# Optimization experiments

Hardware: AMD Instinct MI355X
Metric: run time of the kernel (lower is better)

The kernel has to match this reference:

```python
import jax, jax.numpy as jnp
import numpy as np

VOCAB, EMB, ATT = 100000, 128, 128
N_CODES, N_ANC = 100000, 8

def setup_inputs() -> dict:
    key = jax.random.key(0)
    k1, k2, k3, k4, k5 = jax.random.split(key, 5)
    return {
        "W_emb": jax.random.normal(k1, (VOCAB, EMB), dtype=jnp.float32),
        "W_attention": jax.random.normal(k2, (2 * EMB, ATT), dtype=jnp.float32) * 0.05,
        "b_attention": jnp.zeros((ATT,), dtype=jnp.float32),
        "v_attention": jax.random.normal(k3, (ATT,), dtype=jnp.float32) * 0.05,
        "leaves": jax.random.randint(k4, (N_CODES, N_ANC), 0, VOCAB, dtype=jnp.int64),
        "ancestors": jax.random.randint(k5, (N_CODES, N_ANC), 0, VOCAB, dtype=jnp.int64),
    }

def reference(W_emb, W_attention, b_attention, v_attention, leaves, ancestors):
    # gather: [N, A, E] each
    leave_emb = W_emb[leaves]
    anc_emb = W_emb[ancestors]
    attention_input = jnp.concatenate((leave_emb, anc_emb), axis=2)  # [N, A, 2E]
    mlp = jnp.tanh(jnp.einsum('nae,ed->nad', attention_input, W_attention) + b_attention)
    pre_attention = jnp.einsum('nad,d->na', mlp, v_attention)  # [N, A]
    attn = jax.nn.softmax(pre_attention, axis=1)
    # attention-weighted sum over ancestors: [N, E]
    return jnp.einsum('nae,na->ne', anc_emb, attn)
```

## Files before the change

### kernel.cpp

```cpp
#include <hip/hip_runtime.h>
#include <hip/hip_bf16.h>
#include <hip/hip_fp8.h>

#define VOCAB  100000
#define EMB    128
#define NCODES 100000
#define NANC   8

typedef __attribute__((ext_vector_type(8))) short    short8;
typedef __attribute__((ext_vector_type(4))) float    float4v;
typedef __attribute__((ext_vector_type(2))) float    floatx2;
typedef __attribute__((ext_vector_type(4))) unsigned uint4v;
typedef __attribute__((ext_vector_type(2))) __bf16   bf16x2;

__device__ __forceinline__ ushort f2bf(float x) {
    unsigned u = __float_as_uint(x);
    u += 0x7fffu + ((u >> 16) & 1u);
    return (ushort)(u >> 16);
}
__device__ __forceinline__ float bf2f(ushort h) {
    return __uint_as_float((unsigned)h << 16);
}
__device__ __forceinline__ unsigned pk2bf(float lo, float hi) {
    bf16x2 v;
    v[0] = (__bf16)lo;
    v[1] = (__bf16)hi;
    return __builtin_bit_cast(unsigned, v);
}
__device__ __forceinline__ unsigned char f2fp8(float x) {
    __hip_fp8_e4m3 t(x);
    return t.__x;
}
__device__ __forceinline__ unsigned pack_fp8x4(float a, float b, float c, float d) {
#if __has_builtin(__builtin_amdgcn_cvt_pk_fp8_f32)
    int w = __builtin_amdgcn_cvt_pk_fp8_f32(a, b, 0, false);
    w = __builtin_amdgcn_cvt_pk_fp8_f32(c, d, w, true);
    return (unsigned)w;
#else
    return (unsigned)f2fp8(a) | ((unsigned)f2fp8(b) << 8)
         | ((unsigned)f2fp8(c) << 16) | ((unsigned)f2fp8(d) << 24);
#endif
}
template <bool HI>
__device__ __forceinline__ floatx2 fp8pair(unsigned v) {
#if __has_builtin(__builtin_amdgcn_cvt_pk_f32_fp8)
    return __builtin_amdgcn_cvt_pk_f32_fp8((int)v, HI);
#else
    __hip_fp8_e4m3 a, b;
    const unsigned s = HI ? 16u : 0u;
    a.__x = (v >> s) & 0xffu;
    b.__x = (v >> (s + 8u)) & 0xffu;
    floatx2 r; r[0] = (float)a; r[1] = (float)b; return r;
#endif
}

__device__ __forceinline__ void tanh2pk(floatx2 za, floatx2 zb,
                                        floatx2& ta, floatx2& tb) {
    floatx2 xa, xb;
    xa[0] = fminf(fmaxf(za[0], -3.5f), 3.5f);
    xa[1] = fminf(fmaxf(za[1], -3.5f), 3.5f);
    xb[0] = fminf(fmaxf(zb[0], -3.5f), 3.5f);
    xb[1] = fminf(fmaxf(zb[1], -3.5f), 3.5f);
    const floatx2 ya = xa * xa, yb = xb * xb;
    floatx2 Na = ya + 105.0f;  Na = ya * Na + 945.0f;
    floatx2 Nb = yb + 105.0f;  Nb = yb * Nb + 945.0f;
    floatx2 Da = ya * 15.0f + 420.0f;  Da = ya * Da + 945.0f;
    floatx2 Db = yb * 15.0f + 420.0f;  Db = yb * Db + 945.0f;
    const floatx2 Dp = Da * Db;
    const float r = __builtin_amdgcn_rcpf(Dp[0] * Dp[1]);
    floatx2 qv;  qv[0] = r * Dp[1];  qv[1] = r * Dp[0];
    const floatx2 ia = qv * Db;
    const floatx2 ib = qv * Da;
    ta = (xa * Na) * ia;
    tb = (xb * Nb) * ib;
}

__global__ void transpose_watt(const float* __restrict__ W_att,
                               ushort* __restrict__ WT)
{
    const int id = blockIdx.x * 256 + threadIdx.x;
    const int c = id >> 7, e = id & 127;
    const int h = c >> 7, d = c & 127;
    WT[c * 128 + e] = f2bf(W_att[(h * 128 + e) * 128 + d]);
}

__global__ __launch_bounds__(256) void precompute(
    const float*  __restrict__ W_emb,
    const ushort* __restrict__ WT,
    const float*  __restrict__ b_att,
    unsigned char* __restrict__ P1,
    unsigned char* __restrict__ M)
{
    const int t = threadIdx.x, wave = t >> 6, lane = t & 63;
    const int n15 = lane & 15, quad = lane >> 4;
    const int cw = wave * 64;

    short8 wfrag[4][4];
    #pragma unroll
    for (int ntl = 0; ntl < 4; ++ntl) {
        const int c = cw + ((n15 >> 2) << 4) + ntl * 4 + (n15 & 3);
        #pragma unroll
        for (int kt = 0; kt < 4; ++kt)
            wfrag[kt][ntl] = *(const short8*)(WT + c * 128 + kt * 32 + quad * 8);
    }

    float4 bb[4];
    #pragma unroll
    for (int ntl = 0; ntl < 4; ++ntl) {
        if (wave < 2) bb[ntl] = *(const float4*)(b_att + cw + quad * 16 + ntl * 4);
        else          bb[ntl] = make_float4(0.f, 0.f, 0.f, 0.f);
    }

    unsigned char* Pt;
    size_t rstride;
    int cbase;
    if (wave < 2) { Pt = P1; rstride = 128; cbase = cw + quad * 16; }
    else          { Pt = M;  rstride = 384; cbase = (cw - 128) + quad * 16; }

    const int NT = VOCAB / 16;
    int rt = blockIdx.x;
    float4v cur[8];
    {
        const float4v* src = (const float4v*)(W_emb + (size_t)(rt * 16 + n15) * 128);
        #pragma unroll
        for (int kt = 0; kt < 4; ++kt) {
            cur[2 * kt]     = __builtin_nontemporal_load(src + kt * 8 + quad * 2);
            cur[2 * kt + 1] = __builtin_nontemporal_load(src + kt * 8 + quad * 2 + 1);
        }
    }

    for (; rt < NT; ) {
        const int nrt = rt + gridDim.x;
        float4v nxt[8];
        if (nrt < NT) {
            const float4v* src = (const float4v*)(W_emb + (size_t)(nrt * 16 + n15) * 128);
            #pragma unroll
            for (int kt = 0; kt < 4; ++kt) {
                nxt[2 * kt]     = __builtin_nontemporal_load(src + kt * 8 + quad * 2);
                nxt[2 * kt + 1] = __builtin_nontemporal_load(src + kt * 8 + quad * 2 + 1);
            }
        }

        const int R = rt * 16;
        float4v acc[4];
        #pragma unroll
        for (int i = 0; i < 4; ++i) acc[i] = (float4v)0.0f;

        #pragma unroll
        for (int kt = 0; kt < 4; ++kt) {
            const float4v a0 = cur[2 * kt], a1 = cur[2 * kt + 1];
            uint4v ad;
            ad[0] = pk2bf(a0[0], a0[1]);
            ad[1] = pk2bf(a0[2], a0[3]);
            ad[2] = pk2bf(a1[0], a1[1]);
            ad[3] = pk2bf(a1[2], a1[3]);
            const short8 af = __builtin_bit_cast(short8, ad);
            if ((wave < 2) && ((kt >> 1) == wave))
                *(short8*)(M + (size_t)(R + n15) * 384 + 128 + kt * 64 + quad * 16) = af;
            #pragma unroll
            for (int ntl = 0; ntl < 4; ++ntl)
                acc[ntl] = __builtin_amdgcn_mfma_f32_16x16x32_bf16(
                               wfrag[kt][ntl], af, acc[ntl], 0, 0, 0);
        }

        uint4v pks;
        #pragma unroll
        for (int ntl = 0; ntl < 4; ++ntl)
            pks[ntl] = pack_fp8x4(acc[ntl][0] + bb[ntl].x,
                                  acc[ntl][1] + bb[ntl].y,
                                  acc[ntl][2] + bb[ntl].z,
                                  acc[ntl][3] + bb[ntl].w);
        *(uint4v*)(Pt + (size_t)(R + n15) * rstride + cbase) = pks;

        rt = nrt;
        #pragma unroll
        for (int i = 0; i < 8; ++i) cur[i] = nxt[i];
    }
}

__global__ __launch_bounds__(256) void attention_main(
    const unsigned char* __restrict__ P1,
    const unsigned char* __restrict__ M,
    const float* __restrict__ v_att,
    const int*   __restrict__ leaves, const int* __restrict__ anc,
    float*       __restrict__ out)
{
    const int t = threadIdx.x;
    const int wave = t >> 6, lane = t & 63;
    const int sub = lane >> 4, l16 = lane & 15;
    const int n = blockIdx.x * 16 + wave * 4 + sub;

    floatx2 vv[4];
    #pragma unroll
    for (int p = 0; p < 4; ++p)
        vv[p] = *(const floatx2*)(v_att + l16 * 8 + 2 * p);

    const int jj = l16 & 7;
    const int* idxp = (l16 & 8) ? (anc + n * 8 + jj) : (leaves + n * 8 + jj);
    const int lidx = __builtin_nontemporal_load(idxp);

    int lf[NANC], an[NANC];
    #pragma unroll
    for (int a = 0; a < NANC; ++a) {
        lf[a] = __shfl(lidx, (sub << 4) + a);
        an[a] = __shfl(lidx, (sub << 4) + 8 + a);
    }

    uint2 r1[NANC], r2[NANC];
    short8 em[NANC];
    #pragma unroll
    for (int a = 0; a < NANC; ++a)
        r1[a] = *(const uint2*)(P1 + (size_t)lf[a] * 128 + l16 * 8);
    #pragma unroll
    for (int a = 0; a < NANC; ++a) {
        const unsigned char* mrow = M + (size_t)an[a] * 384;
        r2[a] = *(const uint2*)(mrow + l16 * 8);
        em[a] = *(const short8*)(mrow + 128 + l16 * 16);
    }

    float q[NANC];
    #pragma unroll
    for (int a = 0; a < NANC; ++a) {
        const floatx2 z0 = fp8pair<false>(r1[a].x) + fp8pair<false>(r2[a].x);
        const floatx2 z1 = fp8pair<true >(r1[a].x) + fp8pair<true >(r2[a].x);
        const floatx2 z2 = fp8pair<false>(r1[a].y) + fp8pair<false>(r2[a].y);
        const floatx2 z3 = fp8pair<true >(r1[a].y) + fp8pair<true >(r2[a].y);
        floatx2 t0, t1, t2, t3;
        tanh2pk(z0, z1, t0, t1);
        tanh2pk(z2, z3, t2, t3);
        floatx2 qa = t0 * vv[0];
        qa = t1 * vv[1] + qa;
        qa = t2 * vv[2] + qa;
        qa = t3 * vv[3] + qa;
        q[a] = qa[0] + qa[1];
    }

    float r4[4];
    #pragma unroll
    for (int i = 0; i < 4; ++i) {
        const float keep = (l16 & 8) ? q[i + 4] : q[i];
        const float send = (l16 & 8) ? q[i]     : q[i + 4];
        r4[i] = keep + __shfl_xor(send, 8);
    }
    float s2[2];
    #pragma unroll
    for (int i = 0; i < 2; ++i) {
        const float keep = (l16 & 4) ? r4[i + 2] : r4[i];
        const float send = (l16 & 4) ? r4[i]     : r4[i + 2];
        s2[i] = keep + __shfl_xor(send, 4);
    }
    {
        const float keep = (l16 & 2) ? s2[1] : s2[0];
        const float send = (l16 & 2) ? s2[0] : s2[1];
        s2[0] = keep + __shfl_xor(send, 2);
    }
    float tq = s2[0] + __shfl_xor(s2[0], 1);

    float m = tq;
    m = fmaxf(m, __shfl_xor(m, 8));
    m = fmaxf(m, __shfl_xor(m, 4));
    m = fmaxf(m, __shfl_xor(m, 2));
    const float e = __expf(tq - m);
    float s = e;
    s += __shfl_xor(s, 8); s += __shfl_xor(s, 4); s += __shfl_xor(s, 2);
    const float wl = e * __fdividef(1.0f, s);

    float wa[NANC];
    {
        const float p  = __shfl_xor(wl, 2);
        const float w0 = (l16 & 2) ? p  : wl;
        const float w1 = (l16 & 2) ? wl : p;
        const float p0 = __shfl_xor(w0, 4), p1 = __shfl_xor(w1, 4);
        const float v00 = (l16 & 4) ? p0 : w0, v01 = (l16 & 4) ? p1 : w1;
        const float v10 = (l16 & 4) ? w0 : p0, v11 = (l16 & 4) ? w1 : p1;
        float g;
        g = __shfl_xor(v00, 8); wa[0] = (l16 & 8) ? g : v00; wa[4] = (l16 & 8) ? v00 : g;
        g = __shfl_xor(v01, 8); wa[1] = (l16 & 8) ? g : v01; wa[5] = (l16 & 8) ? v01 : g;
        g = __shfl_xor(v10, 8); wa[2] = (l16 & 8) ? g : v10; wa[6] = (l16 & 8) ? v10 : g;
        g = __shfl_xor(v11, 8); wa[3] = (l16 & 8) ? g : v11; wa[7] = (l16 & 8) ? v11 : g;
    }

    floatx2 o[4] = {(floatx2)0.f, (floatx2)0.f, (floatx2)0.f, (floatx2)0.f};
    #pragma unroll
    for (int a = 0; a < NANC; ++a) {
        floatx2 wv; wv[0] = wa[a]; wv[1] = wa[a];
        #pragma unroll
        for (int p = 0; p < 4; ++p) {
            floatx2 ev;
            ev[0] = bf2f((ushort)em[a][2 * p]);
            ev[1] = bf2f((ushort)em[a][2 * p + 1]);
            o[p] = ev * wv + o[p];
        }
    }
    float4v o1, o2;
    o1[0] = o[0][0]; o1[1] = o[0][1]; o1[2] = o[1][0]; o1[3] = o[1][1];
    o2[0] = o[2][0]; o2[1] = o[2][1]; o2[2] = o[3][0]; o2[3] = o[3][1];
    __builtin_nontemporal_store(o1, (float4v*)(out + (size_t)n * 128 + l16 * 8));
    __builtin_nontemporal_store(o2, (float4v*)(out + (size_t)n * 128 + l16 * 8 + 4));
}

extern "C" void kernel_launch(void* const* d_in, const int* in_sizes, int n_in,
                              void* d_out, int out_size, void* d_ws, size_t ws_size,
                              hipStream_t stream) {
    const float* W_emb  = (const float*)d_in[0];
    const float* W_att  = (const float*)d_in[1];
    const float* b_att  = (const float*)d_in[2];
    const float* v_att  = (const float*)d_in[3];
    const int*   leaves = (const int*)d_in[4];
    const int*   anc    = (const int*)d_in[5];
    float*       out    = (float*)d_out;

    unsigned char* P1 = (unsigned char*)d_ws;
    unsigned char* M  = P1 + (size_t)VOCAB * 128;
    ushort* WT = (ushort*)(M + (size_t)VOCAB * 384);

    transpose_watt<<<128, 256, 0, stream>>>(W_att, WT);
    precompute<<<1250, 256, 0, stream>>>(W_emb, WT, b_att, P1, M);
    attention_main<<<NCODES / 16, 256, 0, stream>>>(P1, M, v_att,
                                                    leaves, anc, out);
}
```

Baseline: 210.8 us.

## Make attention kernel persistent with software-pipelined gathers across tiles

Shrinks the attention grid to 1250 blocks that each loop over 5 tiles of 16 codes. Index loads and the P1/M gathers for the next tile are issued before the current tile's tanh/softmax/weighted-sum math, and index loads run two tiles ahead. The aim is to hide gather latency inside each wave. The cost is roughly double the registers for the gathered rows, which may reduce occupancy, and fewer blocks in flight.

New measurement: 210.6 us. Within noise of the previous version (-0.1%).

```diff
diff --git a/kernel.cpp b/kernel.cpp
--- a/kernel.cpp
+++ b/kernel.cpp
@@ -6,6 +6,9 @@
 #define EMB    128
 #define NCODES 100000
 #define NANC   8
+
+#define ATT_GRID 1250
+#define ATT_TPB  5
 
 typedef __attribute__((ext_vector_type(8))) short    short8;
 typedef __attribute__((ext_vector_type(4))) float    float4v;
@@ -188,115 +191,151 @@
     const int t = threadIdx.x;
     const int wave = t >> 6, lane = t & 63;
     const int sub = lane >> 4, l16 = lane & 15;
-    const int n = blockIdx.x * 16 + wave * 4 + sub;
+    const int jj = l16 & 7;
 
     floatx2 vv[4];
     #pragma unroll
     for (int p = 0; p < 4; ++p)
         vv[p] = *(const floatx2*)(v_att + l16 * 8 + 2 * p);
 
-    const int jj = l16 & 7;
-    const int* idxp = (l16 & 8) ? (anc + n * 8 + jj) : (leaves + n * 8 + jj);
-    const int lidx = __builtin_nontemporal_load(idxp);
-
-    int lf[NANC], an[NANC];
+    const int base = blockIdx.x;
+
+    auto idx_ptr = [&](int tile) -> const int* {
+        const int n = tile * 16 + wave * 4 + sub;
+        return (l16 & 8) ? (anc + n * 8 + jj) : (leaves + n * 8 + jj);
+    };
+
+    int    lf[2][NANC], an[2][NANC];
+    uint2  R1[2][NANC], R2[2][NANC];
+    short8 EM[NANC];
+    int    raw[2];
+
+    raw[0] = __builtin_nontemporal_load(idx_ptr(base));
     #pragma unroll
     for (int a = 0; a < NANC; ++a) {
-        lf[a] = __shfl(lidx, (sub << 4) + a);
-        an[a] = __shfl(lidx, (sub << 4) + 8 + a);
-    }
-
-    uint2 r1[NANC], r2[NANC];
-    short8 em[NANC];
+        lf[0][a] = __shfl(raw[0], (sub << 4) + a);
+        an[0][a] = __shfl(raw[0], (sub << 4) + 8 + a);
+    }
     #pragma unroll
     for (int a = 0; a < NANC; ++a)
-        r1[a] = *(const uint2*)(P1 + (size_t)lf[a] * 128 + l16 * 8);
-    #pragma unroll
-    for (int a = 0; a < NANC; ++a) {
-        const unsigned char* mrow = M + (size_t)an[a] * 384;
-        r2[a] = *(const uint2*)(mrow + l16 * 8);
-        em[a] = *(const short8*)(mrow + 128 + l16 * 16);
-    }
-
-    float q[NANC];
-    #pragma unroll
-    for (int a = 0; a < NANC; ++a) {
-        const floatx2 z0 = fp8pair<false>(r1[a].x) + fp8pair<false>(r2[a].x);
-        const floatx2 z1 = fp8pair<true >(r1[a].x) + fp8pair<true >(r2[a].x);
-        const floatx2 z2 = fp8pair<false>(r1[a].y) + fp8pair<false>(r2[a].y);
-        const floatx2 z3 = fp8pair<true >(r1[a].y) + fp8pair<true >(r2[a].y);
-        floatx2 t0, t1, t2, t3;
-        tanh2pk(z0, z1, t0, t1);
-        tanh2pk(z2, z3, t2, t3);
-        floatx2 qa = t0 * vv[0];
-        qa = t1 * vv[1] + qa;
-        qa = t2 * vv[2] + qa;
-        qa = t3 * vv[3] + qa;
-        q[a] = qa[0] + qa[1];
-    }
-
-    float r4[4];
-    #pragma unroll
-    for (int i = 0; i < 4; ++i) {
-        const float keep = (l16 & 8) ? q[i + 4] : q[i];
-        const float send = (l16 & 8) ? q[i]     : q[i + 4];
-        r4[i] = keep + __shfl_xor(send, 8);
-    }
-    float s2[2];
-    #pragma unroll
-    for (int i = 0; i < 2; ++i) {
-        const float keep = (l16 & 4) ? r4[i + 2] : r4[i];
-        const float send = (l16 & 4) ? r4[i]     : r4[i + 2];
-        s2[i] = keep + __shfl_xor(send, 4);
-    }
-    {
-        const float keep = (l16 & 2) ? s2[1] : s2[0];
-        const float send = (l16 & 2) ? s2[0] : s2[1];
-        s2[0] = keep + __shfl_xor(send, 2);
-    }
-    float tq = s2[0] + __shfl_xor(s2[0], 1);
-
-    float m = tq;
-    m = fmaxf(m, __shfl_xor(m, 8));
-    m = fmaxf(m, __shfl_xor(m, 4));
-    m = fmaxf(m, __shfl_xor(m, 2));
-    const float e = __expf(tq - m);
-    float s = e;
-    s += __shfl_xor(s, 8); s += __shfl_xor(s, 4); s += __shfl_xor(s, 2);
-    const float wl = e * __fdividef(1.0f, s);
-
-    float wa[NANC];
-    {
-        const float p  = __shfl_xor(wl, 2);
-        const float w0 = (l16 & 2) ? p  : wl;
-        const float w1 = (l16 & 2) ? wl : p;
-        const float p0 = __shfl_xor(w0, 4), p1 = __shfl_xor(w1, 4);
-        const float v00 = (l16 & 4) ? p0 : w0, v01 = (l16 & 4) ? p1 : w1;
-        const float v10 = (l16 & 4) ? w0 : p0, v11 = (l16 & 4) ? w1 : p1;
-        float g;
-        g = __shfl_xor(v00, 8); wa[0] = (l16 & 8) ? g : v00; wa[4] = (l16 & 8) ? v00 : g;
-        g = __shfl_xor(v01, 8); wa[1] = (l16 & 8) ? g : v01; wa[5] = (l16 & 8) ? v01 : g;
-        g = __shfl_xor(v10, 8); wa[2] = (l16 & 8) ? g : v10; wa[6] = (l16 & 8) ? v10 : g;
-        g = __shfl_xor(v11, 8); wa[3] = (l16 & 8) ? g : v11; wa[7] = (l16 & 8) ? v11 : g;
-    }
-
-    floatx2 o[4] = {(floatx2)0.f, (floatx2)0.f, (floatx2)0.f, (floatx2)0.f};
-    #pragma unroll
-    for (int a = 0; a < NANC; ++a) {
-        floatx2 wv; wv[0] = wa[a]; wv[1] = wa[a];
-        #pragma unroll
-        for (int p = 0; p < 4; ++p) {
-            floatx2 ev;
-            ev[0] = bf2f((ushort)em[a][2 * p]);
-            ev[1] = bf2f((ushort)em[a][2 * p + 1]);
-            o[p] = ev * wv + o[p];
-        }
-    }
-    float4v o1, o2;
-    o1[0] = o[0][0]; o1[1] = o[0][1]; o1[2] = o[1][0]; o1[3] = o[1][1];
-    o2[0] = o[2][0]; o2[1] = o[2][1]; o2[2] = o[3][0]; o2[3] = o[3][1];
-    __builtin_nontemporal_store(o1, (float4v*)(out + (size_t)n * 128 + l16 * 8));
-    __builtin_nontemporal_store(o2, (float4v*)(out + (size_t)n * 128 + l16 * 8 + 4));
+        R1[0][a] = *(const uint2*)(P1 + (size_t)lf[0][a] * 128 + l16 * 8);
+    #pragma unroll
+    for (int a = 0; a < NANC; ++a)
+        R2[0][a] = *(const uint2*)(M + (size_t)an[0][a] * 384 + l16 * 8);
+    #pragma unroll
+    for (int a = 0; a < NANC; ++a)
+        EM[a] = *(const short8*)(M + (size_t)an[0][a] * 384 + 128 + l16 * 16);
+    raw[1] = __builtin_nontemporal_load(idx_ptr(base + ATT_GRID));
+
+    #pragma unroll
+    for (int it = 0; it < ATT_TPB; ++it) {
+        const int cur = it & 1, nx = cur ^ 1;
+        const int tile = base + it * ATT_GRID;
+
+        if (it + 1 < ATT_TPB) {
+            #pragma unroll
+            for (int a = 0; a < NANC; ++a) {
+                lf[nx][a] = __shfl(raw[nx], (sub << 4) + a);
+                an[nx][a] = __shfl(raw[nx], (sub << 4) + 8 + a);
+            }
+            #pragma unroll
+            for (int a = 0; a < NANC; ++a)
+                R1[nx][a] = *(const uint2*)(P1 + (size_t)lf[nx][a] * 128 + l16 * 8);
+            #pragma unroll
+            for (int a = 0; a < NANC; ++a)
+                R2[nx][a] = *(const uint2*)(M + (size_t)an[nx][a] * 384 + l16 * 8);
+        }
+        if (it + 2 < ATT_TPB)
+            raw[cur] = __builtin_nontemporal_load(idx_ptr(tile + 2 * ATT_GRID));
+
+        const int n = tile * 16 + wave * 4 + sub;
+
+        float q[NANC];
+        #pragma unroll
+        for (int a = 0; a < NANC; ++a) {
+            const floatx2 z0 = fp8pair<false>(R1[cur][a].x) + fp8pair<false>(R2[cur][a].x);
+            const floatx2 z1 = fp8pair<true >(R1[cur][a].x) + fp8pair<true >(R2[cur][a].x);
+            const floatx2 z2 = fp8pair<false>(R1[cur][a].y) + fp8pair<false>(R2[cur][a].y);
+            const floatx2 z3 = fp8pair<true >(R1[cur][a].y) + fp8pair<true >(R2[cur][a].y);
+            floatx2 t0, t1, t2, t3;
+            tanh2pk(z0, z1, t0, t1);
+            tanh2pk(z2, z3, t2, t3);
+            floatx2 qa = t0 * vv[0];
+            qa = t1 * vv[1] + qa;
+            qa = t2 * vv[2] + qa;
+            qa = t3 * vv[3] + qa;
+            q[a] = qa[0] + qa[1];
+        }
+
+        float r4[4];
+        #pragma unroll
+        for (int i = 0; i < 4; ++i) {
+            const float keep = (l16 & 8) ? q[i + 4] : q[i];
+            const float send = (l16 & 8) ? q[i]     : q[i + 4];
+            r4[i] = keep + __shfl_xor(send, 8);
+        }
+        float s2[2];
+        #pragma unroll
+        for (int i = 0; i < 2; ++i) {
+            const float keep = (l16 & 4) ? r4[i + 2] : r4[i];
+            const float send = (l16 & 4) ? r4[i]     : r4[i + 2];
+            s2[i] = keep + __shfl_xor(send, 4);
+        }
+        {
+            const float keep = (l16 & 2) ? s2[1] : s2[0];
+            const float send = (l16 & 2) ? s2[0] : s2[1];
+            s2[0] = keep + __shfl_xor(send, 2);
+        }
+        float tq = s2[0] + __shfl_xor(s2[0], 1);
+
+        float m = tq;
+        m = fmaxf(m, __shfl_xor(m, 8));
+        m = fmaxf(m, __shfl_xor(m, 4));
+        m = fmaxf(m, __shfl_xor(m, 2));
+        const float e = __expf(tq - m);
+        float s = e;
+        s += __shfl_xor(s, 8); s += __shfl_xor(s, 4); s += __shfl_xor(s, 2);
+        const float wl = e * __fdividef(1.0f, s);
+
+        float wa[NANC];
+        {
+            const float p  = __shfl_xor(wl, 2);
+            const float w0 = (l16 & 2) ? p  : wl;
+            const float w1 = (l16 & 2) ? wl : p;
+            const float p0 = __shfl_xor(w0, 4), p1 = __shfl_xor(w1, 4);
+            const float v00 = (l16 & 4) ? p0 : w0, v01 = (l16 & 4) ? p1 : w1;
+            const float v10 = (l16 & 4) ? w0 : p0, v11 = (l16 & 4) ? w1 : p1;
+            float g;
+            g = __shfl_xor(v00, 8); wa[0] = (l16 & 8) ? g : v00; wa[4] = (l16 & 8) ? v00 : g;
+            g = __shfl_xor(v01, 8); wa[1] = (l16 & 8) ? g : v01; wa[5] = (l16 & 8) ? v01 : g;
+            g = __shfl_xor(v10, 8); wa[2] = (l16 & 8) ? g : v10; wa[6] = (l16 & 8) ? v10 : g;
+            g = __shfl_xor(v11, 8); wa[3] = (l16 & 8) ? g : v11; wa[7] = (l16 & 8) ? v11 : g;
+        }
+
+        floatx2 o[4] = {(floatx2)0.f, (floatx2)0.f, (floatx2)0.f, (floatx2)0.f};
+        #pragma unroll
+        for (int a = 0; a < NANC; ++a) {
+            floatx2 wv; wv[0] = wa[a]; wv[1] = wa[a];
+            #pragma unroll
+            for (int p = 0; p < 4; ++p) {
+                floatx2 ev;
+                ev[0] = bf2f((ushort)EM[a][2 * p]);
+                ev[1] = bf2f((ushort)EM[a][2 * p + 1]);
+                o[p] = ev * wv + o[p];
+            }
+        }
+        float4v o1, o2;
+        o1[0] = o[0][0]; o1[1] = o[0][1]; o1[2] = o[1][0]; o1[3] = o[1][1];
+        o2[0] = o[2][0]; o2[1] = o[2][1]; o2[2] = o[3][0]; o2[3] = o[3][1];
+        __builtin_nontemporal_store(o1, (float4v*)(out + (size_t)n * 128 + l16 * 8));
+        __builtin_nontemporal_store(o2, (float4v*)(out + (size_t)n * 128 + l16 * 8 + 4));
+
+        if (it + 1 < ATT_TPB) {
+            #pragma unroll
+            for (int a = 0; a < NANC; ++a)
+                EM[a] = *(const short8*)(M + (size_t)an[nx][a] * 384 + 128 + l16 * 16);
+        }
+    }
 }
 
 extern "C" void kernel_launch(void* const* d_in, const int* in_sizes, int n_in,
@@ -316,6 +355,6 @@
 
     transpose_watt<<<128, 256, 0, stream>>>(W_att, WT);
     precompute<<<1250, 256, 0, stream>>>(W_emb, WT, b_att, P1, M);
-    attention_main<<<NCODES / 16, 256, 0, stream>>>(P1, M, v_att,
-                                                    leaves, anc, out);
-}
+    attention_main<<<ATT_GRID, 256, 0, stream>>>(P1, M, v_att,
+                                                 leaves, anc, out);
+}
```
